# Kernel optimization log

Hardware: AMD Instinct MI355X
Metric: run time of the kernel (lower is better)

The kernel has to match this reference:

```python
import jax, jax.numpy as jnp
import numpy as np

B, N, C, H, R = 64, 197, 768, 12, 24  # batch, tokens (196 patches + cls), dim, heads, lora rank
D = C // H  # head_dim = 64


def make_rel_index(ws=(14, 14)):
    Wh, Ww = ws
    coords = np.stack(np.meshgrid(np.arange(Wh), np.arange(Ww), indexing='ij'))  # [2,Wh,Ww]
    cf = coords.reshape(2, -1)
    rel = (cf[:, :, None] - cf[:, None, :]).transpose(1, 2, 0).astype(np.int64)
    rel[:, :, 0] += Wh - 1
    rel[:, :, 1] += Ww - 1
    rel[:, :, 0] *= 2 * Ww - 1
    num_rel = (2 * Wh - 1) * (2 * Ww - 1) + 3
    idx = np.zeros((Wh * Ww + 1,) * 2, dtype=np.int32)
    idx[1:, 1:] = rel.sum(-1)
    idx[0, :] = num_rel - 3
    idx[:, 0] = num_rel - 2
    idx[0, 0] = num_rel - 1
    return idx


def setup_inputs() -> dict:
    key = jax.random.key(0)
    ks = jax.random.split(key, 16)
    s = 0.02
    # 1D rotary table over 196 patch positions, interleaved pairs over head_dim
    pos = np.arange(N - 1, dtype=np.float32)
    inv_freq = 1.0 / (10000.0 ** (np.arange(0, D, 2, dtype=np.float32) / D))  # [D/2]
    ang = np.repeat(pos[:, None] * inv_freq[None, :], 2, axis=-1)  # [196, 64]
    return {
        'x': jax.random.normal(ks[0], (B, N, C), jnp.float32),
        'qkv_w': jax.random.normal(ks[1], (3 * C, C), jnp.float32) * s,
        'q_bias': jax.random.normal(ks[2], (C,), jnp.float32) * s,
        'v_bias': jax.random.normal(ks[3], (C,), jnp.float32) * s,
        'lora_q_a': jax.random.normal(ks[4], (R, C), jnp.float32) * s,
        'lora_q_b': jax.random.normal(ks[5], (C, R), jnp.float32) * s,
        'lora_k_a': jax.random.normal(ks[6], (R, C), jnp.float32) * s,
        'lora_k_b': jax.random.normal(ks[7], (C, R), jnp.float32) * s,
        'lora_v_a': jax.random.normal(ks[8], (R, C), jnp.float32) * s,
        'lora_v_b': jax.random.normal(ks[9], (C, R), jnp.float32) * s,
        'rel_table': jax.random.normal(ks[10], (732, H), jnp.float32) * s,
        'rope_cos': jnp.asarray(np.cos(ang)),
        'rope_sin': jnp.asarray(np.sin(ang)),
        'proj_w': jax.random.normal(ks[11], (C, C), jnp.float32) * s,
        'proj_b': jax.random.normal(ks[12], (C,), jnp.float32) * s,
        'rel_index': jnp.asarray(make_rel_index((14, 14))),
    }


def _rope(t, cos, sin):
    # t: [B,H,M,D]; cos/sin: [M,D]; EVA rotate_half over interleaved pairs
    tp = t.reshape(t.shape[:-1] + (D // 2, 2))
    rot = jnp.stack((-tp[..., 1], tp[..., 0]), axis=-1).reshape(t.shape)
    return t * cos + rot * sin


def reference(x, qkv_w, q_bias, v_bias, lora_q_a, lora_q_b, lora_k_a, lora_k_b,
              lora_v_a, lora_v_b, rel_table, rope_cos, rope_sin, proj_w, proj_b, rel_index):
    b, n, c = x.shape
    h = rel_table.shape[1]
    d = c // h
    scale = d ** -0.5
    bias = jnp.concatenate([q_bias, jnp.zeros_like(v_bias), v_bias])
    qkv = x @ qkv_w.T + bias  # [B,N,3C]
    lora = jnp.concatenate([(x @ lora_q_a.T) @ lora_q_b.T,
                            (x @ lora_k_a.T) @ lora_k_b.T,
                            (x @ lora_v_a.T) @ lora_v_b.T], axis=-1)
    qkv = (qkv + lora).reshape(b, n, 3, h, d).transpose(2, 0, 3, 1, 4)  # [3,B,H,N,D]
    q, k, v = qkv[0], qkv[1], qkv[2]
    # rope on non-cls tokens only
    q = jnp.concatenate([q[:, :, :1], _rope(q[:, :, 1:], rope_cos, rope_sin)], axis=2)
    k = jnp.concatenate([k[:, :, :1], _rope(k[:, :, 1:], rope_cos, rope_sin)], axis=2)
    attn = jnp.einsum('bhqd,bhkd->bhqk', (q * scale).astype(jnp.float32), k.astype(jnp.float32))
    rpb = rel_table[rel_index.reshape(-1)].reshape(n, n, h).transpose(2, 0, 1)  # [H,N,N]
    attn = attn + rpb[None].astype(attn.dtype)
    attn = jax.nn.softmax(attn, axis=-1).astype(x.dtype)
    out = jnp.einsum('bhqk,bhkd->bhqd', attn, v).transpose(0, 2, 1, 3).reshape(b, n, c)
    return out @ proj_w.T + proj_b
```

## Files before the change

### kernel.cpp

```cpp
#include <hip/hip_runtime.h>
#include <stdint.h>

typedef __bf16 bf16x8 __attribute__((ext_vector_type(8)));
typedef short short8 __attribute__((ext_vector_type(8)));
typedef float f32x4 __attribute__((ext_vector_type(4)));
typedef float f32x4v __attribute__((ext_vector_type(4)));
typedef unsigned short u16x4 __attribute__((ext_vector_type(4)));

#define DEV static __device__ __forceinline__

DEV float b2f(unsigned short u) {
    union { float f; unsigned v; } x; x.v = ((unsigned)u) << 16; return x.f;
}
DEV unsigned short f2b(float f) {
    union { float f; unsigned v; } x; x.f = f;
    unsigned r = x.v + 0x7fffu + ((x.v >> 16) & 1u);
    return (unsigned short)(r >> 16);
}
DEV f32x4 zero4() { f32x4 z; z[0]=0.f; z[1]=0.f; z[2]=0.f; z[3]=0.f; return z; }

#define MFMA16(a, b, c) __builtin_amdgcn_mfma_f32_16x16x32_bf16(a, b, c, 0, 0, 0)

DEV void gload16(const unsigned short* g, unsigned short* l) {
    __builtin_amdgcn_global_load_lds(
        (const __attribute__((address_space(1))) void*)g,
        (__attribute__((address_space(3))) void*)l,
        16, 0, 0);
}

__global__ __launch_bounds__(256)
void prep_kernel(const float* __restrict__ x, unsigned short* __restrict__ xb,
                 const float* __restrict__ pw, unsigned short* __restrict__ pwb,
                 const float* __restrict__ qkvw,
                 const float* __restrict__ qa, const float* __restrict__ qbb,
                 const float* __restrict__ ka, const float* __restrict__ kb,
                 const float* __restrict__ va, const float* __restrict__ vbb,
                 unsigned short* __restrict__ W,
                 const float* __restrict__ rtab, const int* __restrict__ ridx,
                 float* __restrict__ rpb)
{
    const int S0 = 9682944 / 4;
    const int S1 = 589824 / 4;
    const int S2 = 2304 * 768;
    const int S3 = 12 * 197 * 224;
    const int total = S0 + S1 + S2 + S3;
    for (int i = blockIdx.x * 256 + threadIdx.x; i < total; i += gridDim.x * 256) {
        if (i < S0) {
            f32x4v v = *(const f32x4v*)(x + (size_t)i * 4);
            u16x4 o;
            #pragma unroll
            for (int j = 0; j < 4; ++j) o[j] = f2b(v[j]);
            *(u16x4*)(xb + (size_t)i * 4) = o;
        } else if (i < S0 + S1) {
            const int k = i - S0;
            f32x4v v = *(const f32x4v*)(pw + (size_t)k * 4);
            u16x4 o;
            #pragma unroll
            for (int j = 0; j < 4; ++j) o[j] = f2b(v[j]);
            *(u16x4*)(pwb + (size_t)k * 4) = o;
        } else if (i < S0 + S1 + S2) {
            const int idx = i - S0 - S1;
            const int o = idx / 768;
            const int c = idx - o * 768;
            const int sec = o / 768;
            const int ol = o - sec * 768;
            const float* a_ = (sec == 0) ? qa : (sec == 1 ? ka : va);
            const float* b_ = (sec == 0) ? qbb : (sec == 1 ? kb : vbb);
            float acc = qkvw[idx];
            #pragma unroll
            for (int r = 0; r < 24; ++r)
                acc += b_[ol * 24 + r] * a_[r * 768 + c];
            W[idx] = f2b(acc);
        } else {
            const int idx = i - S0 - S1 - S2;
            const int h = idx / (197 * 224);
            const int rem = idx - h * 197 * 224;
            const int qq = rem / 224;
            const int kk = rem - qq * 224;
            float v = 0.f;
            if (kk < 197) v = rtab[ridx[qq * 197 + kk] * 12 + h];
            rpb[idx] = v;
        }
    }
}

template<int EPI>
__global__ __launch_bounds__(256, 2)
void gemm_bt(const unsigned short* __restrict__ A, const unsigned short* __restrict__ Bw,
             int M, int Nout, int ntn,
             const float* __restrict__ qb, const float* __restrict__ vb,
             const float* __restrict__ rcos, const float* __restrict__ rsin,
             unsigned short* __restrict__ oq, unsigned short* __restrict__ ok,
             unsigned short* __restrict__ ov,
             const float* __restrict__ pb, float* __restrict__ o2)
{
    constexpr int K = 768, TK = 24;
    __shared__ __align__(16) unsigned short lA[3][128 * 32];
    __shared__ __align__(16) unsigned short lB[3][128 * 32];
    const int tid = threadIdx.x;
    const int lane = tid & 63, wave = tid >> 6;

    const int nwg = gridDim.x;
    const int qq_ = nwg >> 3, rr_ = nwg & 7;
    const int xcd = blockIdx.x & 7, orig8 = blockIdx.x >> 3;
    const int wgid = (xcd < rr_ ? xcd * (qq_ + 1) : rr_ * (qq_ + 1) + (xcd - rr_) * qq_) + orig8;
    const int mt = wgid / ntn, nt = wgid - mt * ntn;
    const int m0 = mt * 128, n0 = nt * 128;
    const int wm = (wave >> 1) * 64, wn = (wave & 1) * 64;

    int srow[2], sunit[2];
    #pragma unroll
    for (int j = 0; j < 2; ++j) {
        const int P = wave * 2048 + j * 1024 + lane * 16;
        const int L = P ^ (((P >> 7) & 7) << 4);
        srow[j] = L >> 6;
        sunit[j] = (L >> 4) & 3;
    }

    const int laneA = lane & 15, laneQ = lane >> 4;
    int aoff[4], boff[4];
    #pragma unroll
    for (int i = 0; i < 4; ++i) {
        int lb = (wm + i * 16 + laneA) * 64 + laneQ * 16;
        aoff[i] = (lb ^ (((lb >> 7) & 7) << 4)) >> 1;
        lb = (wn + i * 16 + laneA) * 64 + laneQ * 16;
        boff[i] = (lb ^ (((lb >> 7) & 7) << 4)) >> 1;
    }

    f32x4 acc[4][4];
    #pragma unroll
    for (int i = 0; i < 4; ++i)
        #pragma unroll
        for (int j = 0; j < 4; ++j) acc[i][j] = zero4();

    auto stage = [&](int kt, int bsel) {
        const int k0 = kt << 5;
        #pragma unroll
        for (int j = 0; j < 2; ++j) {
            int gr = m0 + srow[j]; if (gr > M - 1) gr = M - 1;
            gload16(A + (size_t)gr * K + k0 + sunit[j] * 8,
                    (unsigned short*)lA[bsel] + wave * 1024 + j * 512);
        }
        #pragma unroll
        for (int j = 0; j < 2; ++j) {
            const int br = n0 + srow[j];
            gload16(Bw + (size_t)br * K + k0 + sunit[j] * 8,
                    (unsigned short*)lB[bsel] + wave * 1024 + j * 512);
        }
    };

    stage(0, 0);
    stage(1, 1);
    asm volatile("s_waitcnt vmcnt(4)" ::: "memory");
    __builtin_amdgcn_s_barrier();

    #pragma unroll
    for (int t = 0; t < TK; ++t) {
        if (t + 2 < TK) stage(t + 2, (t + 2) % 3);
        const unsigned short* aT = (const unsigned short*)lA[t % 3];
        const unsigned short* bT = (const unsigned short*)lB[t % 3];
        bf16x8 af[4], bfr[4];
        #pragma unroll
        for (int i = 0; i < 4; ++i) af[i] = *(const bf16x8*)(aT + aoff[i]);
        #pragma unroll
        for (int i = 0; i < 4; ++i) bfr[i] = *(const bf16x8*)(bT + boff[i]);
        #pragma unroll
        for (int mi = 0; mi < 4; ++mi)
            #pragma unroll
            for (int ni = 0; ni < 4; ++ni)
                acc[mi][ni] = MFMA16(af[mi], bfr[ni], acc[mi][ni]);
        if (t + 1 < TK) {
            if (t + 2 < TK) asm volatile("s_waitcnt vmcnt(4)" ::: "memory");
            else            asm volatile("s_waitcnt vmcnt(0)" ::: "memory");
            __builtin_amdgcn_s_barrier();
        }
    }

    #pragma unroll
    for (int mi = 0; mi < 4; ++mi) {
        #pragma unroll
        for (int j = 0; j < 4; ++j) {
            const int m = m0 + wm + mi * 16 + (lane >> 4) * 4 + j;
            const bool mv = (m < M);
            int b_ = 0, n = 0;
            if constexpr (EPI == 1) { b_ = m / 197; n = m - b_ * 197; }
            #pragma unroll
            for (int ni = 0; ni < 4; ++ni) {
                const int o = n0 + wn + ni * 16 + laneA;
                float val = acc[mi][ni][j];
                if constexpr (EPI == 1) {
                    const int sec = o / 768;
                    const int oc = o - sec * 768;
                    const int d = oc & 63;
                    if (sec == 0) val += qb[oc];
                    else if (sec == 2) val += vb[oc];
                    if (sec < 2 && n > 0) {
                        const float part = __shfl_xor(val, 1, 64);
                        const float co = rcos[(n - 1) * 64 + d];
                        const float si = rsin[(n - 1) * 64 + d];
                        val = val * co + ((o & 1) ? part : -part) * si;
                    }
                    if (sec == 0) val *= 0.125f;
                    if (mv) {
                        const int h = oc >> 6;
                        unsigned short* dst = (sec == 0) ? oq : (sec == 1 ? ok : ov);
                        dst[((size_t)(b_ * 12 + h) * 197 + n) * 64 + d] = f2b(val);
                    }
                } else {
                    val += pb[o];
                    if (mv) o2[(size_t)m * Nout + o] = val;
                }
            }
        }
    }
}

__global__ __launch_bounds__(256)
void attn_kernel(const unsigned short* __restrict__ qs, const unsigned short* __restrict__ ksrc,
                 const unsigned short* __restrict__ vsrc, const float* __restrict__ rpb,
                 unsigned short* __restrict__ aout)
{
    __shared__ __align__(16) unsigned short Pl[64 * 232];
    __shared__ __align__(16) unsigned short Vt[64 * 232];
    __shared__ float inv_s[64];
    const int chunk = blockIdx.x;
    const int h = blockIdx.y;
    const int b = blockIdx.z;
    const int tid = threadIdx.x, lane = tid & 63, wave = tid >> 6;
    const size_t base = ((size_t)(b * 12 + h)) * 197 * 64;
    const unsigned short* q = qs + base;
    const unsigned short* kp = ksrc + base;
    const unsigned short* vp = vsrc + base;

    if (tid < 224) {
        const int kc = tid;
        if (kc < 197) {
            #pragma unroll
            for (int d0 = 0; d0 < 8; ++d0) {
                short8 vv = *(const short8*)(vp + kc * 64 + d0 * 8);
                #pragma unroll
                for (int i = 0; i < 8; ++i)
                    Vt[(d0 * 8 + i) * 232 + kc] = (unsigned short)vv[i];
            }
        } else {
            #pragma unroll
            for (int dd = 0; dd < 64; ++dd) Vt[dd * 232 + kc] = 0;
        }
    }

    const int laneA = lane & 15;
    const int laneK = (lane >> 4) * 8;
    const int q0 = chunk * 64 + wave * 16;

    int qr = q0 + laneA; if (qr > 196) qr = 196;
    const bf16x8 qf0 = *(const bf16x8*)(q + qr * 64 + laneK);
    const bf16x8 qf1 = *(const bf16x8*)(q + qr * 64 + 32 + laneK);

    f32x4 s[13];
    #pragma unroll
    for (int kt = 0; kt < 13; ++kt) {
        int kr = kt * 16 + laneA; if (kr > 196) kr = 196;
        const bf16x8 kf0 = *(const bf16x8*)(kp + kr * 64 + laneK);
        const bf16x8 kf1 = *(const bf16x8*)(kp + kr * 64 + 32 + laneK);
        f32x4 c = zero4();
        c = MFMA16(qf0, kf0, c);
        c = MFMA16(qf1, kf1, c);
        s[kt] = c;
    }

    const int rowb = (lane >> 4) * 4;
    float mx[4] = {-1e30f, -1e30f, -1e30f, -1e30f};
    #pragma unroll
    for (int kt = 0; kt < 13; ++kt) {
        const int kc = kt * 16 + laneA;
        #pragma unroll
        for (int j = 0; j < 4; ++j) {
            int qg = q0 + rowb + j; if (qg > 196) qg = 196;
            float v = s[kt][j] + rpb[((size_t)h * 197 + qg) * 224 + kc];
            if (kc > 196) v = -1e30f;
            s[kt][j] = v;
            mx[j] = fmaxf(mx[j], v);
        }
    }
    #pragma unroll
    for (int off = 1; off < 16; off <<= 1)
        #pragma unroll
        for (int j = 0; j < 4; ++j) mx[j] = fmaxf(mx[j], __shfl_xor(mx[j], off, 64));
    float sm[4] = {0.f, 0.f, 0.f, 0.f};
    #pragma unroll
    for (int kt = 0; kt < 13; ++kt)
        #pragma unroll
        for (int j = 0; j < 4; ++j) {
            const float e = __expf(s[kt][j] - mx[j]);
            s[kt][j] = e;
            sm[j] += e;
        }
    #pragma unroll
    for (int off = 1; off < 16; off <<= 1)
        #pragma unroll
        for (int j = 0; j < 4; ++j) sm[j] += __shfl_xor(sm[j], off, 64);
    if (laneA == 0) {
        #pragma unroll
        for (int j = 0; j < 4; ++j) inv_s[wave * 16 + rowb + j] = 1.0f / sm[j];
    }
    #pragma unroll
    for (int kt = 0; kt < 13; ++kt) {
        const int kc = kt * 16 + laneA;
        #pragma unroll
        for (int j = 0; j < 4; ++j) {
            const int lr = wave * 16 + rowb + j;
            Pl[lr * 232 + kc] = (kc <= 196) ? f2b(s[kt][j]) : (unsigned short)0;
        }
    }
    #pragma unroll
    for (int j = 0; j < 4; ++j)
        Pl[(wave * 16 + rowb + j) * 232 + 208 + laneA] = 0;

    __syncthreads();

    f32x4 oacc[4];
    #pragma unroll
    for (int i = 0; i < 4; ++i) oacc[i] = zero4();
    #pragma unroll
    for (int ks2 = 0; ks2 < 7; ++ks2) {
        const bf16x8 pf = *(const bf16x8*)(Pl + (wave * 16 + laneA) * 232 + ks2 * 32 + laneK);
        #pragma unroll
        for (int ni = 0; ni < 4; ++ni) {
            const bf16x8 vf = *(const bf16x8*)(Vt + (ni * 16 + laneA) * 232 + ks2 * 32 + laneK);
            oacc[ni] = MFMA16(pf, vf, oacc[ni]);
        }
    }
    #pragma unroll
    for (int ni = 0; ni < 4; ++ni)
        #pragma unroll
        for (int j = 0; j < 4; ++j) {
            const int lq = wave * 16 + rowb + j;
            const int qg = chunk * 64 + lq;
            if (qg < 197) {
                const int d = ni * 16 + laneA;
                const float val = oacc[ni][j] * inv_s[lq];
                aout[((size_t)b * 197 + qg) * 768 + h * 64 + d] = f2b(val);
            }
        }
}

extern "C" void kernel_launch(void* const* d_in, const int* in_sizes, int n_in,
                              void* d_out, int out_size, void* d_ws, size_t ws_size,
                              hipStream_t stream)
{
    const float* x    = (const float*)d_in[0];
    const float* qkvw = (const float*)d_in[1];
    const float* qb   = (const float*)d_in[2];
    const float* vb   = (const float*)d_in[3];
    const float* lqa  = (const float*)d_in[4];
    const float* lqb  = (const float*)d_in[5];
    const float* lka  = (const float*)d_in[6];
    const float* lkb  = (const float*)d_in[7];
    const float* lva  = (const float*)d_in[8];
    const float* lvb  = (const float*)d_in[9];
    const float* rtab = (const float*)d_in[10];
    const float* rcos = (const float*)d_in[11];
    const float* rsin = (const float*)d_in[12];
    const float* pw   = (const float*)d_in[13];
    const float* pb   = (const float*)d_in[14];
    const int* ridx   = (const int*)d_in[15];

    const int M = 64 * 197;
    const size_t XSZ = (size_t)M * 768;
    const size_t QSZ = (size_t)64 * 12 * 197 * 64;

    char* ws = (char*)d_ws;
    unsigned short* xb   = (unsigned short*)ws;
    unsigned short* pwb  = xb + XSZ;
    unsigned short* Weff = pwb + (size_t)768 * 768;
    unsigned short* qsb  = Weff + (size_t)2304 * 768;
    unsigned short* ksb  = qsb + QSZ;
    unsigned short* vsb  = ksb + QSZ;
    float* rpb           = (float*)(vsb + QSZ);
    unsigned short* aout = (unsigned short*)(rpb + (size_t)12 * 197 * 224);

    prep_kernel<<<2048, 256, 0, stream>>>(x, xb, pw, pwb, qkvw,
                                          lqa, lqb, lka, lkb, lva, lvb, Weff,
                                          rtab, ridx, rpb);
    gemm_bt<1><<<99 * 18, 256, 0, stream>>>(xb, Weff, M, 2304, 18,
                                            qb, vb, rcos, rsin, qsb, ksb, vsb,
                                            nullptr, nullptr);
    attn_kernel<<<dim3(4, 12, 64), 256, 0, stream>>>(qsb, ksb, vsb, rpb, aout);
    gemm_bt<2><<<99 * 6, 256, 0, stream>>>(aout, pwb, M, 768, 6,
                                           nullptr, nullptr, nullptr, nullptr,
                                           nullptr, nullptr, nullptr,
                                           pb, (float*)d_out);
}
```

Baseline: 239.8 us.

## Write V transposed from QKV GEMM epilogue and DMA it into attention LDS

The QKV GEMM epilogue now stores V in a transposed [b,h,d,224] layout, and the prep kernel zeroes the padding columns 197..223. The attention kernel no longer transposes V through scalar LDS stores; it copies the pre-transposed tile with global_load_lds. This moves the transpose cost out of every attention block (four chunks per head each redid it) and into scattered 2-byte stores in the GEMM epilogue. The V LDS stride drops from 232 to 224, which may add bank conflicts on the PV MFMA reads.

Measured after the change: 252.3 us. +5.2%, slower.

```diff
diff --git a/kernel.cpp b/kernel.cpp
--- a/kernel.cpp
+++ b/kernel.cpp
@@ -37,13 +37,14 @@
                  const float* __restrict__ va, const float* __restrict__ vbb,
                  unsigned short* __restrict__ W,
                  const float* __restrict__ rtab, const int* __restrict__ ridx,
-                 float* __restrict__ rpb)
+                 float* __restrict__ rpb, unsigned short* __restrict__ vtb)
 {
     const int S0 = 9682944 / 4;
     const int S1 = 589824 / 4;
     const int S2 = 2304 * 768;
     const int S3 = 12 * 197 * 224;
-    const int total = S0 + S1 + S2 + S3;
+    const int S4 = 64 * 12 * 64 * 32;
+    const int total = S0 + S1 + S2 + S3 + S4;
     for (int i = blockIdx.x * 256 + threadIdx.x; i < total; i += gridDim.x * 256) {
         if (i < S0) {
             f32x4v v = *(const f32x4v*)(x + (size_t)i * 4);
@@ -71,7 +72,7 @@
             for (int r = 0; r < 24; ++r)
                 acc += b_[ol * 24 + r] * a_[r * 768 + c];
             W[idx] = f2b(acc);
-        } else {
+        } else if (i < S0 + S1 + S2 + S3) {
             const int idx = i - S0 - S1 - S2;
             const int h = idx / (197 * 224);
             const int rem = idx - h * 197 * 224;
@@ -80,6 +81,10 @@
             float v = 0.f;
             if (kk < 197) v = rtab[ridx[qq * 197 + kk] * 12 + h];
             rpb[idx] = v;
+        } else {
+            const int idx = i - S0 - S1 - S2 - S3;
+            const int rest = idx >> 5;
+            vtb[(size_t)rest * 224 + 192 + (idx & 31)] = 0;
         }
     }
 }
@@ -203,8 +208,12 @@
                     if (sec == 0) val *= 0.125f;
                     if (mv) {
                         const int h = oc >> 6;
-                        unsigned short* dst = (sec == 0) ? oq : (sec == 1 ? ok : ov);
-                        dst[((size_t)(b_ * 12 + h) * 197 + n) * 64 + d] = f2b(val);
+                        if (sec == 2) {
+                            ov[((size_t)(b_ * 12 + h) * 64 + d) * 224 + n] = f2b(val);
+                        } else {
+                            unsigned short* dst = (sec == 0) ? oq : ok;
+                            dst[((size_t)(b_ * 12 + h) * 197 + n) * 64 + d] = f2b(val);
+                        }
                     }
                 } else {
                     val += pb[o];
@@ -217,11 +226,11 @@
 
 __global__ __launch_bounds__(256)
 void attn_kernel(const unsigned short* __restrict__ qs, const unsigned short* __restrict__ ksrc,
-                 const unsigned short* __restrict__ vsrc, const float* __restrict__ rpb,
+                 const unsigned short* __restrict__ vtg, const float* __restrict__ rpb,
                  unsigned short* __restrict__ aout)
 {
     __shared__ __align__(16) unsigned short Pl[64 * 232];
-    __shared__ __align__(16) unsigned short Vt[64 * 232];
+    __shared__ __align__(16) unsigned short Vt[64 * 224];
     __shared__ float inv_s[64];
     const int chunk = blockIdx.x;
     const int h = blockIdx.y;
@@ -230,21 +239,13 @@
     const size_t base = ((size_t)(b * 12 + h)) * 197 * 64;
     const unsigned short* q = qs + base;
     const unsigned short* kp = ksrc + base;
-    const unsigned short* vp = vsrc + base;
-
-    if (tid < 224) {
-        const int kc = tid;
-        if (kc < 197) {
-            #pragma unroll
-            for (int d0 = 0; d0 < 8; ++d0) {
-                short8 vv = *(const short8*)(vp + kc * 64 + d0 * 8);
-                #pragma unroll
-                for (int i = 0; i < 8; ++i)
-                    Vt[(d0 * 8 + i) * 232 + kc] = (unsigned short)vv[i];
-            }
-        } else {
-            #pragma unroll
-            for (int dd = 0; dd < 64; ++dd) Vt[dd * 232 + kc] = 0;
+
+    {
+        const unsigned short* vt = vtg + (size_t)(b * 12 + h) * 14336;
+        #pragma unroll
+        for (int i = 0; i < 7; ++i) {
+            const int inst = wave * 7 + i;
+            gload16(vt + inst * 512 + lane * 8, Vt + inst * 512);
         }
     }
 
@@ -326,7 +327,7 @@
         const bf16x8 pf = *(const bf16x8*)(Pl + (wave * 16 + laneA) * 232 + ks2 * 32 + laneK);
         #pragma unroll
         for (int ni = 0; ni < 4; ++ni) {
-            const bf16x8 vf = *(const bf16x8*)(Vt + (ni * 16 + laneA) * 232 + ks2 * 32 + laneK);
+            const bf16x8 vf = *(const bf16x8*)(Vt + (ni * 16 + laneA) * 224 + ks2 * 32 + laneK);
             oacc[ni] = MFMA16(pf, vf, oacc[ni]);
         }
     }
@@ -368,6 +369,7 @@
     const int M = 64 * 197;
     const size_t XSZ = (size_t)M * 768;
     const size_t QSZ = (size_t)64 * 12 * 197 * 64;
+    const size_t VTSZ = (size_t)64 * 12 * 64 * 224;
 
     char* ws = (char*)d_ws;
     unsigned short* xb   = (unsigned short*)ws;
@@ -375,17 +377,17 @@
     unsigned short* Weff = pwb + (size_t)768 * 768;
     unsigned short* qsb  = Weff + (size_t)2304 * 768;
     unsigned short* ksb  = qsb + QSZ;
-    unsigned short* vsb  = ksb + QSZ;
-    float* rpb           = (float*)(vsb + QSZ);
+    unsigned short* vtb  = ksb + QSZ;
+    float* rpb           = (float*)(vtb + VTSZ);
     unsigned short* aout = (unsigned short*)(rpb + (size_t)12 * 197 * 224);
 
     prep_kernel<<<2048, 256, 0, stream>>>(x, xb, pw, pwb, qkvw,
                                           lqa, lqb, lka, lkb, lva, lvb, Weff,
-                                          rtab, ridx, rpb);
+                                          rtab, ridx, rpb, vtb);
     gemm_bt<1><<<99 * 18, 256, 0, stream>>>(xb, Weff, M, 2304, 18,
-                                            qb, vb, rcos, rsin, qsb, ksb, vsb,
+                                            qb, vb, rcos, rsin, qsb, ksb, vtb,
                                             nullptr, nullptr);
-    attn_kernel<<<dim3(4, 12, 64), 256, 0, stream>>>(qsb, ksb, vsb, rpb, aout);
+    attn_kernel<<<dim3(4, 12, 64), 256, 0, stream>>>(qsb, ksb, vtb, rpb, aout);
     gemm_bt<2><<<99 * 6, 256, 0, stream>>>(aout, pwb, M, 768, 6,
                                            nullptr, nullptr, nullptr, nullptr,
                                            nullptr, nullptr, nullptr,
```
